# Kernel optimization log

Hardware: AMD Instinct MI355X
Metric: run time of the kernel (lower is better)

## Reference

```python
import jax, jax.numpy as jnp
import numpy as np

NUM_HEADS = 8
ATTN_LEN = 5


def setup_inputs() -> dict:
    rng = jax.random.key(0)
    ks = jax.random.split(rng, 10)
    B, T, D = 2, 4096, 1024
    H, HD = NUM_HEADS, D // NUM_HEADS
    n = lambda k, shape, scale=1.0: jax.random.normal(k, shape, jnp.float32) * scale
    return {
        "query": n(ks[0], (B, T, D)),
        "key": n(ks[1], (B, T, D)),
        "value": n(ks[2], (B, T, D)),
        "Wq": n(ks[3], (D, D), 0.02),
        "bq": jnp.zeros((D,), jnp.float32),
        "Wk": n(ks[4], (D, D), 0.02),
        "bk": jnp.zeros((D,), jnp.float32),
        "Wv": n(ks[5], (D, D), 0.02),
        "bv": jnp.zeros((D,), jnp.float32),
        "Er": n(ks[6], (H, HD, ATTN_LEN)),
        "layer": 1,
    }


def _forward(query, key, value, Wq, bq, Wk, bk, Wv, bv, Er, layer):
    B, T, D = query.shape
    H = NUM_HEADS
    HD = D // H
    dil = 2 ** layer
    pad = dil * (ATTN_LEN // 2)
    Tp = T + 2 * pad

    # torch nn.Linear: y = x @ W^T + b ; reshape to [B, H, T, HD]
    q = (query @ Wq.T + bq).reshape(B, T, H, HD).transpose(0, 2, 1, 3)
    k = (key @ Wk.T + bk).reshape(B, T, H, HD).transpose(0, 2, 1, 3)
    v = (value @ Wv.T + bv).reshape(B, T, H, HD).transpose(0, 2, 1, 3)

    # head-group source mapping + shifts (note k head 7 reuses k head 6, per source)
    src_k = jnp.array([0, 1, 2, 3, 4, 5, 6, 6])
    src_v = jnp.array([0, 1, 2, 3, 4, 5, 6, 7])
    shifts = jnp.array([0, 0, 0, 0, -2, -1, 1, 2])

    # kv_roll equivalence: window slot j at time t for shift s reads
    # padded[(t + (s + j) * dil) mod Tp]  (torch.roll wraparound included)
    t_idx = jnp.arange(T)
    j_idx = jnp.arange(ATTN_LEN)
    idx = (t_idx[None, :, None] + (shifts[:, None, None] + j_idx[None, None, :]) * dil) % Tp  # [H,T,L]

    def windows(x, src):
        xp = jnp.pad(x, ((0, 0), (0, 0), (pad, pad), (0, 0)))[:, src]  # [B,H,Tp,HD]
        g = jnp.take_along_axis(xp, idx.reshape(1, H, T * ATTN_LEN, 1), axis=2)
        return g.reshape(B, H, T, ATTN_LEN, HD)

    kw = windows(k, src_k)  # [B,H,T,L,HD]
    vw = windows(v, src_v)

    qk = jnp.einsum('bhtd,bhtjd->bhtj', q, kw)            # [B,H,T,L]
    mask = jnp.where(qk == 0.0, -jnp.inf, 0.0)            # zero dot product => padding
    qer = jnp.einsum('bhtd,hdj->bhtj', q, Er)             # relative positional bias
    attn = jax.nn.softmax((qk + qer) / np.sqrt(HD).astype(np.float32) + mask, axis=-1)
    out = jnp.einsum('bhtj,bhtjd->bhtd', attn, vw)        # [B,H,T,HD]
    out = out.transpose(0, 2, 1, 3).reshape(B, T, D)
    return out, attn[:, :, :, None, :]                     # attn shaped [B,H,T,1,L] like torch


def reference(query, key, value, Wq, bq, Wk, bk, Wv, bv, Er, layer):
    return _forward(query, key, value, Wq, bq, Wk, bk, Wv, bv, Er, layer)
```

## Files before the change

### kernel.cpp

```cpp
#include <hip/hip_runtime.h>
#include <hip/hip_bf16.h>

constexpr int B_ = 2, T_ = 4096, D_ = 1024, H_ = 8, HD_ = 128, L_ = 5;
constexpr int M_ = B_ * T_;
constexpr int K_ = D_;
constexpr int N_ = D_;

typedef __attribute__((ext_vector_type(8))) __bf16 bf16x8;
typedef __attribute__((ext_vector_type(4))) float f32x4;

__device__ __constant__ int c_srck[8]  = {0, 1, 2, 3, 4, 5, 6, 6};
__device__ __constant__ int c_shift[8] = {0, 0, 0, 0, -2, -1, 1, 2};

__device__ __forceinline__ void gload_lds16(const void* g, void* l) {
    __builtin_amdgcn_global_load_lds(
        (__attribute__((address_space(1))) void*)g,
        (__attribute__((address_space(3))) void*)l, 16, 0, 0);
}

__global__ __launch_bounds__(256) void qkv_gemm(
    const float* __restrict__ query,
    const float* __restrict__ key,
    const float* __restrict__ value,
    const float* __restrict__ Wq,
    const float* __restrict__ bq,
    const float* __restrict__ Wk,
    const float* __restrict__ bk,
    const float* __restrict__ Wv,
    const float* __restrict__ bv,
    __hip_bfloat16* __restrict__ qout,
    __hip_bfloat16* __restrict__ kout,
    __hip_bfloat16* __restrict__ vout)
{
    const int z = blockIdx.z;
    const float* A    = (z == 0) ? query : (z == 1) ? key : value;
    const float* W    = (z == 0) ? Wq    : (z == 1) ? Wk  : Wv;
    const float* bias = (z == 0) ? bq    : (z == 1) ? bk  : bv;
    __hip_bfloat16* C = (z == 0) ? qout  : (z == 1) ? kout : vout;

    __shared__ __align__(16) float As[128 * 32];
    __shared__ __align__(16) float Bs[128 * 32];

    const int tid  = threadIdx.x;
    const int wave = tid >> 6;
    const int lane = tid & 63;
    const int m0 = blockIdx.x * 128;
    const int n0 = blockIdx.y * 128;

    const int wm = (wave >> 1) * 64;
    const int wn = (wave & 1) * 64;

    f32x4 acc[4][4];
#pragma unroll
    for (int i = 0; i < 4; ++i)
#pragma unroll
        for (int j = 0; j < 4; ++j)
            acc[i][j] = (f32x4){0.f, 0.f, 0.f, 0.f};

    const int srow = lane >> 3;
    const int lcg  = (lane & 7) ^ srow;
    const int gcol = lcg * 4;

    const int fr  = lane & 15;
    const int r7  = fr & 7;
    const int cgA = (lane >> 4) * 2;
    const int pcg0 = (cgA)     ^ r7;
    const int pcg1 = (cgA ^ 1) ^ r7;

    for (int k0 = 0; k0 < K_; k0 += 32) {
#pragma unroll
        for (int r = 0; r < 4; ++r) {
            const int issue = wave + r * 4;
            const int row = issue * 8 + srow;
            gload_lds16(A + (size_t)(m0 + row) * K_ + k0 + gcol,
                        (void*)(As + issue * 256));
            gload_lds16(W + (size_t)(n0 + row) * K_ + k0 + gcol,
                        (void*)(Bs + issue * 256));
        }
        __syncthreads();

        bf16x8 af[4], bf[4];
#pragma unroll
        for (int i = 0; i < 4; ++i) {
            const float* ap = As + (wm + i * 16 + fr) * 32;
            f32x4 a0 = *(const f32x4*)(const void*)(ap + pcg0 * 4);
            f32x4 a1 = *(const f32x4*)(const void*)(ap + pcg1 * 4);
            const float* bp = Bs + (wn + i * 16 + fr) * 32;
            f32x4 b0 = *(const f32x4*)(const void*)(bp + pcg0 * 4);
            f32x4 b1 = *(const f32x4*)(const void*)(bp + pcg1 * 4);
#pragma unroll
            for (int e = 0; e < 4; ++e) {
                af[i][e]     = (__bf16)a0[e];
                af[i][e + 4] = (__bf16)a1[e];
                bf[i][e]     = (__bf16)b0[e];
                bf[i][e + 4] = (__bf16)b1[e];
            }
        }
#pragma unroll
        for (int i = 0; i < 4; ++i)
#pragma unroll
            for (int j = 0; j < 4; ++j)
                acc[i][j] = __builtin_amdgcn_mfma_f32_16x16x32_bf16(
                    af[i], bf[j], acc[i][j], 0, 0, 0);
        __syncthreads();
    }

    const int col_l = lane & 15;
    const int row_l = (lane >> 4) * 4;
#pragma unroll
    for (int j = 0; j < 4; ++j) {
        const int n = n0 + wn + j * 16 + col_l;
        const float bval = bias[n];
#pragma unroll
        for (int i = 0; i < 4; ++i) {
            const int m = m0 + wm + i * 16 + row_l;
#pragma unroll
            for (int r = 0; r < 4; ++r)
                C[(size_t)(m + r) * N_ + n] = __float2bfloat16(acc[i][j][r] + bval);
        }
    }
}

__global__ __launch_bounds__(256) void attn_kernel(
    const __hip_bfloat16* __restrict__ qp,
    const __hip_bfloat16* __restrict__ kp,
    const __hip_bfloat16* __restrict__ vp,
    const float* __restrict__ Er,
    const int* __restrict__ layer_p,
    float* __restrict__ out,
    float* __restrict__ attn_out)
{
    const int layer = *layer_p;
    const int dil = 1 << layer;
    const int pad = dil * (L_ / 2);
    const int Tp  = T_ + 2 * pad;

    const int tid = threadIdx.x;
    const int g = tid >> 4;
    const int s = tid & 15;

    const int rid = blockIdx.x * 16 + g;
    const int t  = rid & (T_ - 1);
    const int bh = rid >> 12;
    const int h  = bh & (H_ - 1);
    const int b  = bh >> 3;

    const int srck  = c_srck[h];
    const int shift = c_shift[h];

    const size_t qbase = (size_t)(b * T_ + t) * D_ + h * HD_ + s * 8;
    float qf[8];
    {
        bf16x8 qv = *(const bf16x8*)(const void*)(qp + qbase);
#pragma unroll
        for (int e = 0; e < 8; ++e) qf[e] = (float)qv[e];
    }

    float er[8][5];
    {
        const float* ep = Er + ((size_t)h * HD_ + s * 8) * L_;
#pragma unroll
        for (int c = 0; c < 10; ++c) {
            f32x4 ev = *(const f32x4*)(const void*)(ep + c * 4);
#pragma unroll
            for (int e = 0; e < 4; ++e) {
                const int flat = c * 4 + e;
                er[flat / 5][flat % 5] = ev[e];
            }
        }
    }

    float logit[5];
    bool  valid[5];
    int   origs[5];
#pragma unroll
    for (int j = 0; j < 5; ++j) {
        int tt = t + (shift + j) * dil;
        if (tt < 0)   tt += Tp;
        if (tt >= Tp) tt -= Tp;
        const int orig = tt - pad;
        const bool ok = (orig >= 0) && (orig < T_);
        valid[j] = ok;
        origs[j] = ok ? orig : 0;

        bf16x8 kv = *(const bf16x8*)(const void*)(
            kp + (size_t)(b * T_ + origs[j]) * D_ + srck * HD_ + s * 8);
        float comb = 0.f;
#pragma unroll
        for (int e = 0; e < 8; ++e) comb += qf[e] * (float)kv[e];
        if (!ok) comb = 0.f;
#pragma unroll
        for (int e = 0; e < 8; ++e) comb += qf[e] * er[e][j];

#pragma unroll
        for (int off = 1; off < 16; off <<= 1)
            comb += __shfl_xor(comb, off, 16);

        logit[j] = ok ? comb * 0.08838834764831845f : -INFINITY;
    }

    float mx = logit[0];
#pragma unroll
    for (int j = 1; j < 5; ++j) mx = fmaxf(mx, logit[j]);
    float p[5], sum = 0.f;
#pragma unroll
    for (int j = 0; j < 5; ++j) {
        p[j] = valid[j] ? __expf(logit[j] - mx) : 0.f;
        sum += p[j];
    }
    const float inv = 1.f / sum;

    float o[8] = {0.f, 0.f, 0.f, 0.f, 0.f, 0.f, 0.f, 0.f};
#pragma unroll
    for (int j = 0; j < 5; ++j) {
        bf16x8 vv = *(const bf16x8*)(const void*)(
            vp + (size_t)(b * T_ + origs[j]) * D_ + h * HD_ + s * 8);
        const float w = p[j] * inv;
#pragma unroll
        for (int e = 0; e < 8; ++e) o[e] += w * (float)vv[e];
    }

    f32x4 o0 = (f32x4){o[0], o[1], o[2], o[3]};
    f32x4 o1 = (f32x4){o[4], o[5], o[6], o[7]};
    *(f32x4*)(void*)(out + qbase)     = o0;
    *(f32x4*)(void*)(out + qbase + 4) = o1;

    if (s < 5)
        attn_out[((size_t)(b * H_ + h) * T_ + t) * L_ + s] = p[s] * inv;
}

extern "C" void kernel_launch(void* const* d_in, const int* in_sizes, int n_in,
                              void* d_out, int out_size, void* d_ws, size_t ws_size,
                              hipStream_t stream) {
    const float* query = (const float*)d_in[0];
    const float* key   = (const float*)d_in[1];
    const float* value = (const float*)d_in[2];
    const float* Wq    = (const float*)d_in[3];
    const float* bq    = (const float*)d_in[4];
    const float* Wk    = (const float*)d_in[5];
    const float* bk    = (const float*)d_in[6];
    const float* Wv    = (const float*)d_in[7];
    const float* bv    = (const float*)d_in[8];
    const float* Er    = (const float*)d_in[9];
    const int*   layer = (const int*)d_in[10];

    float* out  = (float*)d_out;
    float* attn = out + (size_t)B_ * T_ * D_;

    __hip_bfloat16* qp = (__hip_bfloat16*)d_ws;
    __hip_bfloat16* kp = qp + (size_t)M_ * N_;
    __hip_bfloat16* vp = kp + (size_t)M_ * N_;

    qkv_gemm<<<dim3(M_ / 128, N_ / 128, 3), 256, 0, stream>>>(
        query, key, value, Wq, bq, Wk, bk, Wv, bv, qp, kp, vp);

    attn_kernel<<<dim3(B_ * H_ * T_ / 16), 256, 0, stream>>>(
        qp, kp, vp, Er, layer, out, attn);
}
```

Before: 268.0 us.

## Pre-convert inputs to bf16 and tile attention windows through shared memory

Adds a conversion kernel that turns the fp32 activations and weights into bf16 once, so the QKV GEMM loads half the bytes and skips per-tile conversion. It also rewrites the attention kernel to stage a contiguous block of K/V rows per (time-block, head, batch) in LDS and reuse them across the 64 queries, with each query handled by 4 threads. The conversion pass costs an extra read and write of all inputs and needs a larger workspace; an fp32 GEMM fallback runs when the workspace is too small. If the dilation is large, clamping the window count at NSMAX could go out of range.

```diff
diff --git a/kernel.cpp b/kernel.cpp
--- a/kernel.cpp
+++ b/kernel.cpp
@@ -5,6 +5,8 @@
 constexpr int M_ = B_ * T_;
 constexpr int K_ = D_;
 constexpr int N_ = D_;
+constexpr int TB_ = 64;
+constexpr int NSMAX_ = 96;
 
 typedef __attribute__((ext_vector_type(8))) __bf16 bf16x8;
 typedef __attribute__((ext_vector_type(4))) float f32x4;
@@ -18,7 +20,121 @@
         (__attribute__((address_space(3))) void*)l, 16, 0, 0);
 }
 
-__global__ __launch_bounds__(256) void qkv_gemm(
+__global__ __launch_bounds__(256) void cvt_kernel(
+    const float* __restrict__ q,  const float* __restrict__ k,  const float* __restrict__ v,
+    const float* __restrict__ wq, const float* __restrict__ wk, const float* __restrict__ wv,
+    __hip_bfloat16* __restrict__ qb,  __hip_bfloat16* __restrict__ kb,  __hip_bfloat16* __restrict__ vb,
+    __hip_bfloat16* __restrict__ wqb, __hip_bfloat16* __restrict__ wkb, __hip_bfloat16* __restrict__ wvb)
+{
+    const int y = blockIdx.y;
+    const float* src;
+    __hip_bfloat16* dst;
+    size_t idx;
+    if (blockIdx.x < 4096) {
+        src = (y == 0) ? q : (y == 1) ? k : v;
+        dst = (y == 0) ? qb : (y == 1) ? kb : vb;
+        idx = ((size_t)blockIdx.x * 256 + threadIdx.x) * 8;
+    } else {
+        src = (y == 0) ? wq : (y == 1) ? wk : wv;
+        dst = (y == 0) ? wqb : (y == 1) ? wkb : wvb;
+        idx = ((size_t)(blockIdx.x - 4096) * 256 + threadIdx.x) * 8;
+    }
+    f32x4 a = *(const f32x4*)(const void*)(src + idx);
+    f32x4 b = *(const f32x4*)(const void*)(src + idx + 4);
+    bf16x8 o;
+#pragma unroll
+    for (int e = 0; e < 4; ++e) { o[e] = (__bf16)a[e]; o[e + 4] = (__bf16)b[e]; }
+    *(bf16x8*)(void*)(dst + idx) = o;
+}
+
+__global__ __launch_bounds__(256) void qkv_gemm_bf16(
+    const __hip_bfloat16* __restrict__ qb,
+    const __hip_bfloat16* __restrict__ kb,
+    const __hip_bfloat16* __restrict__ vb,
+    const __hip_bfloat16* __restrict__ wqb,
+    const __hip_bfloat16* __restrict__ wkb,
+    const __hip_bfloat16* __restrict__ wvb,
+    const float* __restrict__ bq,
+    const float* __restrict__ bk,
+    const float* __restrict__ bv,
+    __hip_bfloat16* __restrict__ qout,
+    __hip_bfloat16* __restrict__ kout,
+    __hip_bfloat16* __restrict__ vout)
+{
+    const int z = blockIdx.z;
+    const __hip_bfloat16* A = (z == 0) ? qb  : (z == 1) ? kb  : vb;
+    const __hip_bfloat16* W = (z == 0) ? wqb : (z == 1) ? wkb : wvb;
+    const float* bias       = (z == 0) ? bq  : (z == 1) ? bk  : bv;
+    __hip_bfloat16* C       = (z == 0) ? qout : (z == 1) ? kout : vout;
+
+    __shared__ __align__(16) __hip_bfloat16 As[128 * 32];
+    __shared__ __align__(16) __hip_bfloat16 Bs[128 * 32];
+
+    const int tid  = threadIdx.x;
+    const int wave = tid >> 6;
+    const int lane = tid & 63;
+    const int m0 = blockIdx.x * 128;
+    const int n0 = blockIdx.y * 128;
+    const int wm = (wave >> 1) * 64;
+    const int wn = (wave & 1) * 64;
+
+    f32x4 acc[4][4];
+#pragma unroll
+    for (int i = 0; i < 4; ++i)
+#pragma unroll
+        for (int j = 0; j < 4; ++j)
+            acc[i][j] = (f32x4){0.f, 0.f, 0.f, 0.f};
+
+    const int srow = lane >> 2;
+    const int scol = (lane & 3) * 8;
+
+    const int fr = lane & 15;
+    const int fk = (lane >> 4) * 8;
+
+    for (int k0 = 0; k0 < K_; k0 += 32) {
+#pragma unroll
+        for (int r = 0; r < 2; ++r) {
+            const int issue = wave + r * 4;
+            const int row = issue * 16 + srow;
+            gload_lds16(A + (size_t)(m0 + row) * K_ + k0 + scol,
+                        (void*)(As + issue * 512));
+            gload_lds16(W + (size_t)(n0 + row) * K_ + k0 + scol,
+                        (void*)(Bs + issue * 512));
+        }
+        __syncthreads();
+
+        bf16x8 af[4], bf[4];
+#pragma unroll
+        for (int i = 0; i < 4; ++i) {
+            af[i] = *(const bf16x8*)(const void*)(As + (wm + i * 16 + fr) * 32 + fk);
+            bf[i] = *(const bf16x8*)(const void*)(Bs + (wn + i * 16 + fr) * 32 + fk);
+        }
+#pragma unroll
+        for (int i = 0; i < 4; ++i)
+#pragma unroll
+            for (int j = 0; j < 4; ++j)
+                acc[i][j] = __builtin_amdgcn_mfma_f32_16x16x32_bf16(
+                    af[i], bf[j], acc[i][j], 0, 0, 0);
+        __syncthreads();
+    }
+
+    const int col_l = lane & 15;
+    const int row_l = (lane >> 4) * 4;
+#pragma unroll
+    for (int j = 0; j < 4; ++j) {
+        const int n = n0 + wn + j * 16 + col_l;
+        const float bval = bias[n];
+#pragma unroll
+        for (int i = 0; i < 4; ++i) {
+            const int m = m0 + wm + i * 16 + row_l;
+#pragma unroll
+            for (int r = 0; r < 4; ++r)
+                C[(size_t)(m + r) * N_ + n] = __float2bfloat16(acc[i][j][r] + bval);
+        }
+    }
+}
+
+__global__ __launch_bounds__(256) void qkv_gemm_f32(
     const float* __restrict__ query,
     const float* __restrict__ key,
     const float* __restrict__ value,
@@ -46,7 +162,6 @@
     const int lane = tid & 63;
     const int m0 = blockIdx.x * 128;
     const int n0 = blockIdx.y * 128;
-
     const int wm = (wave >> 1) * 64;
     const int wn = (wave & 1) * 64;
 
@@ -130,103 +245,128 @@
     float* __restrict__ out,
     float* __restrict__ attn_out)
 {
-    const int layer = *layer_p;
-    const int dil = 1 << layer;
-    const int pad = dil * (L_ / 2);
-    const int Tp  = T_ + 2 * pad;
+    const int dil = 1 << (*layer_p);
+    int NS = TB_ + 4 * dil;
+    if (NS > NSMAX_) NS = NSMAX_;
 
     const int tid = threadIdx.x;
-    const int g = tid >> 4;
-    const int s = tid & 15;
-
-    const int rid = blockIdx.x * 16 + g;
-    const int t  = rid & (T_ - 1);
-    const int bh = rid >> 12;
-    const int h  = bh & (H_ - 1);
-    const int b  = bh >> 3;
-
+    const int t0 = blockIdx.x * TB_;
+    const int h  = blockIdx.y;
+    const int b  = blockIdx.z;
+    const int shift = c_shift[h];
     const int srck  = c_srck[h];
-    const int shift = c_shift[h];
-
-    const size_t qbase = (size_t)(b * T_ + t) * D_ + h * HD_ + s * 8;
-    float qf[8];
-    {
-        bf16x8 qv = *(const bf16x8*)(const void*)(qp + qbase);
-#pragma unroll
-        for (int e = 0; e < 8; ++e) qf[e] = (float)qv[e];
-    }
-
-    float er[8][5];
-    {
-        const float* ep = Er + ((size_t)h * HD_ + s * 8) * L_;
-#pragma unroll
-        for (int c = 0; c < 10; ++c) {
-            f32x4 ev = *(const f32x4*)(const void*)(ep + c * 4);
-#pragma unroll
-            for (int e = 0; e < 4; ++e) {
-                const int flat = c * 4 + e;
-                er[flat / 5][flat % 5] = ev[e];
+    const int off_lo = (shift - 2) * dil;
+
+    __shared__ __align__(16) __hip_bfloat16 Ks[NSMAX_ * 128];
+    __shared__ __align__(16) __hip_bfloat16 Vs[NSMAX_ * 128];
+    __shared__ __align__(16) float ErT[5][128];
+
+    for (int i = tid; i < 640; i += 256) {
+        const int d = i / 5, j = i - d * 5;
+        ErT[j][d] = Er[(size_t)h * 640 + i];
+    }
+
+    const int sr = tid >> 4;
+    const int sc = tid & 15;
+    for (int i0 = 0; i0 < NS; i0 += 16) {
+        const int i = i0 + sr;
+        if (i < NS) {
+            const int r = t0 + off_lo + i;
+            bf16x8 kv8 = (bf16x8){0, 0, 0, 0, 0, 0, 0, 0};
+            bf16x8 vv8 = (bf16x8){0, 0, 0, 0, 0, 0, 0, 0};
+            if (r >= 0 && r < T_) {
+                kv8 = *(const bf16x8*)(const void*)(
+                    kp + (size_t)(b * T_ + r) * D_ + srck * HD_ + sc * 8);
+                vv8 = *(const bf16x8*)(const void*)(
+                    vp + (size_t)(b * T_ + r) * D_ + h * HD_ + sc * 8);
             }
-        }
-    }
-
-    float logit[5];
+            const int pc = sc ^ (i & 3);
+            *(bf16x8*)(void*)(Ks + i * 128 + pc * 8) = kv8;
+            *(bf16x8*)(void*)(Vs + i * 128 + pc * 8) = vv8;
+        }
+    }
+    __syncthreads();
+
+    const int lr = tid >> 2;
+    const int ld = tid & 3;
+    const int t  = t0 + lr;
+    const size_t qoff = (size_t)(b * T_ + t) * D_ + h * HD_ + ld * 32;
+
+    float qf[32];
+#pragma unroll
+    for (int c = 0; c < 4; ++c) {
+        bf16x8 qv = *(const bf16x8*)(const void*)(qp + qoff + c * 8);
+#pragma unroll
+        for (int e = 0; e < 8; ++e) qf[c * 8 + e] = (float)qv[e];
+    }
+
+    float lg[5];
     bool  valid[5];
-    int   origs[5];
+    int   irow[5];
 #pragma unroll
     for (int j = 0; j < 5; ++j) {
-        int tt = t + (shift + j) * dil;
-        if (tt < 0)   tt += Tp;
-        if (tt >= Tp) tt -= Tp;
-        const int orig = tt - pad;
-        const bool ok = (orig >= 0) && (orig < T_);
-        valid[j] = ok;
-        origs[j] = ok ? orig : 0;
-
-        bf16x8 kv = *(const bf16x8*)(const void*)(
-            kp + (size_t)(b * T_ + origs[j]) * D_ + srck * HD_ + s * 8);
-        float comb = 0.f;
-#pragma unroll
-        for (int e = 0; e < 8; ++e) comb += qf[e] * (float)kv[e];
-        if (!ok) comb = 0.f;
-#pragma unroll
-        for (int e = 0; e < 8; ++e) comb += qf[e] * er[e][j];
-
-#pragma unroll
-        for (int off = 1; off < 16; off <<= 1)
-            comb += __shfl_xor(comb, off, 16);
-
-        logit[j] = ok ? comb * 0.08838834764831845f : -INFINITY;
-    }
-
-    float mx = logit[0];
-#pragma unroll
-    for (int j = 1; j < 5; ++j) mx = fmaxf(mx, logit[j]);
-    float p[5], sum = 0.f;
+        const int i = lr + j * dil;
+        irow[j] = i;
+        const int orig = t + (shift + j - 2) * dil;
+        valid[j] = (orig >= 0) && (orig < T_);
+
+        float s = 0.f;
+#pragma unroll
+        for (int c = 0; c < 4; ++c) {
+            const int pc = (ld * 4 + c) ^ (i & 3);
+            bf16x8 kk = *(const bf16x8*)(const void*)(Ks + i * 128 + pc * 8);
+#pragma unroll
+            for (int e = 0; e < 8; ++e) s += qf[c * 8 + e] * (float)kk[e];
+        }
+        if (!valid[j]) s = 0.f;
+#pragma unroll
+        for (int c = 0; c < 8; ++c) {
+            f32x4 ev = *(const f32x4*)(const void*)(&ErT[j][ld * 32 + c * 4]);
+#pragma unroll
+            for (int e = 0; e < 4; ++e) s += qf[c * 4 + e] * ev[e];
+        }
+        s += __shfl_xor(s, 1, 4);
+        s += __shfl_xor(s, 2, 4);
+        lg[j] = valid[j] ? s * 0.08838834764831845f : -INFINITY;
+    }
+
+    float mx = lg[0];
+#pragma unroll
+    for (int j = 1; j < 5; ++j) mx = fmaxf(mx, lg[j]);
+    float w[5], sum = 0.f;
 #pragma unroll
     for (int j = 0; j < 5; ++j) {
-        p[j] = valid[j] ? __expf(logit[j] - mx) : 0.f;
-        sum += p[j];
+        w[j] = valid[j] ? __expf(lg[j] - mx) : 0.f;
+        sum += w[j];
     }
     const float inv = 1.f / sum;
-
-    float o[8] = {0.f, 0.f, 0.f, 0.f, 0.f, 0.f, 0.f, 0.f};
+#pragma unroll
+    for (int j = 0; j < 5; ++j) w[j] *= inv;
+
+    float o[32];
+#pragma unroll
+    for (int m = 0; m < 32; ++m) o[m] = 0.f;
 #pragma unroll
     for (int j = 0; j < 5; ++j) {
-        bf16x8 vv = *(const bf16x8*)(const void*)(
-            vp + (size_t)(b * T_ + origs[j]) * D_ + h * HD_ + s * 8);
-        const float w = p[j] * inv;
-#pragma unroll
-        for (int e = 0; e < 8; ++e) o[e] += w * (float)vv[e];
-    }
-
-    f32x4 o0 = (f32x4){o[0], o[1], o[2], o[3]};
-    f32x4 o1 = (f32x4){o[4], o[5], o[6], o[7]};
-    *(f32x4*)(void*)(out + qbase)     = o0;
-    *(f32x4*)(void*)(out + qbase + 4) = o1;
-
-    if (s < 5)
-        attn_out[((size_t)(b * H_ + h) * T_ + t) * L_ + s] = p[s] * inv;
+        const int i = irow[j];
+#pragma unroll
+        for (int c = 0; c < 4; ++c) {
+            const int pc = (ld * 4 + c) ^ (i & 3);
+            bf16x8 vv = *(const bf16x8*)(const void*)(Vs + i * 128 + pc * 8);
+#pragma unroll
+            for (int e = 0; e < 8; ++e) o[c * 8 + e] += w[j] * (float)vv[e];
+        }
+    }
+
+#pragma unroll
+    for (int c = 0; c < 8; ++c) {
+        f32x4 ov = (f32x4){o[c * 4], o[c * 4 + 1], o[c * 4 + 2], o[c * 4 + 3]};
+        *(f32x4*)(void*)(out + qoff + c * 4) = ov;
+    }
+
+    const size_t abase = ((size_t)(b * H_ + h) * T_ + t) * L_;
+    attn_out[abase + ld] = w[ld];
+    if (ld == 0) attn_out[abase + 4] = w[4];
 }
 
 extern "C" void kernel_launch(void* const* d_in, const int* in_sizes, int n_in,
@@ -247,13 +387,40 @@
     float* out  = (float*)d_out;
     float* attn = out + (size_t)B_ * T_ * D_;
 
-    __hip_bfloat16* qp = (__hip_bfloat16*)d_ws;
-    __hip_bfloat16* kp = qp + (size_t)M_ * N_;
-    __hip_bfloat16* vp = kp + (size_t)M_ * N_;
-
-    qkv_gemm<<<dim3(M_ / 128, N_ / 128, 3), 256, 0, stream>>>(
-        query, key, value, Wq, bq, Wk, bk, Wv, bv, qp, kp, vp);
-
-    attn_kernel<<<dim3(B_ * H_ * T_ / 16), 256, 0, stream>>>(
-        qp, kp, vp, Er, layer, out, attn);
-}
+    const size_t SA = (size_t)M_ * K_;
+    const size_t SW = (size_t)N_ * K_;
+    const size_t SP = (size_t)M_ * N_;
+    const size_t need = (3 * SA + 3 * SW + 3 * SP) * sizeof(__hip_bfloat16);
+
+    char* ws = (char*)d_ws;
+    if (ws_size >= need) {
+        __hip_bfloat16* qb  = (__hip_bfloat16*)ws;
+        __hip_bfloat16* kb  = qb + SA;
+        __hip_bfloat16* vb  = kb + SA;
+        __hip_bfloat16* wqb = vb + SA;
+        __hip_bfloat16* wkb = wqb + SW;
+        __hip_bfloat16* wvb = wkb + SW;
+        __hip_bfloat16* qp  = wvb + SW;
+        __hip_bfloat16* kp  = qp + SP;
+        __hip_bfloat16* vp  = kp + SP;
+
+        cvt_kernel<<<dim3(4608, 3), 256, 0, stream>>>(
+            query, key, value, Wq, Wk, Wv, qb, kb, vb, wqb, wkb, wvb);
+
+        qkv_gemm_bf16<<<dim3(M_ / 128, N_ / 128, 3), 256, 0, stream>>>(
+            qb, kb, vb, wqb, wkb, wvb, bq, bk, bv, qp, kp, vp);
+
+        attn_kernel<<<dim3(T_ / TB_, H_, B_), 256, 0, stream>>>(
+            qp, kp, vp, Er, layer, out, attn);
+    } else {
+        __hip_bfloat16* qp = (__hip_bfloat16*)ws;
+        __hip_bfloat16* kp = qp + SP;
+        __hip_bfloat16* vp = kp + SP;
+
+        qkv_gemm_f32<<<dim3(M_ / 128, N_ / 128, 3), 256, 0, stream>>>(
+            query, key, value, Wq, bq, Wk, bk, Wv, bv, qp, kp, vp);
+
+        attn_kernel<<<dim3(T_ / TB_, H_, B_), 256, 0, stream>>>(
+            qp, kp, vp, Er, layer, out, attn);
+    }
+}
```

New measurement: 254.5 us. 5.1% less time.
